# Kernel tuning notes

Hardware: AMD Instinct MI355X
Metric: run time of the kernel (lower is better)

## Reference

```python
import jax, jax.numpy as jnp
import numpy as np

N, D, P = 4096, 1024, 2048
TAU, ALPHA = 0.2, 0.8
GAMMA_EX, GAMMA_IN = 2.0, 1.6
EPS = 1e-8


def _cos_sim(e):
    # F.cosine_similarity(e[:,None], e[None,:], dim=2) == normalized rows matmul
    n = jnp.linalg.norm(e, axis=1, keepdims=True)
    en = e / jnp.maximum(n, EPS)
    return en @ en.T  # [N, N]


def setup_inputs() -> dict:
    key = jax.random.key(0)
    embeddings = jax.random.normal(key, (N, D), dtype=jnp.float32)
    # positive pairs: (0,1),(2,3),... (arange fill)
    pp = np.arange(2 * P).reshape(P, 2)
    pos_partner = np.arange(N)
    pos_partner[pp[:, 0]] = pp[:, 1]
    pos_partner[pp[:, 1]] = pp[:, 0]
    # negative pairs = all ordered (i,j), i!=j, minus ordered positive tuples,
    # enumerated row-major (deterministic stand-in for torch's set order).
    pos_m = np.zeros((N, N), dtype=bool)
    pos_m[pp[:, 0], pp[:, 1]] = True
    neg_m = ~np.eye(N, dtype=bool) & ~pos_m
    ii, jj = np.nonzero(neg_m)  # row-major order
    neg_partner = np.arange(N)
    neg_partner[ii] = jj
    neg_partner[jj] = ii  # processed[j] = ... overwrites after
    return {
        "embeddings": embeddings,
        "positive_pairs": jnp.asarray(pp, jnp.int32),
        "pos_partner": jnp.asarray(pos_partner, jnp.int32),
        "neg_partner": jnp.asarray(neg_partner, jnp.int32),
    }


def reference(embeddings, positive_pairs, pos_partner, neg_partner):
    pi, pj = positive_pairs[:, 0], positive_pairs[:, 1]
    # Beta(gamma,gamma) scalar mixing coefficients (dim_mixing=False)
    lam_pos = jax.random.beta(jax.random.key(1), GAMMA_EX, GAMMA_EX) + 1.0  # 'ex'
    lam_neg = jax.random.beta(jax.random.key(2), GAMMA_IN, GAMMA_IN)        # 'in'

    orig = _cos_sim(embeddings)
    hp = _cos_sim(lam_pos * embeddings + (1.0 - lam_pos) * embeddings[pos_partner])
    hn = _cos_sim(lam_neg * embeddings + (1.0 - lam_neg) * embeddings[neg_partner])

    eye = jnp.eye(N, dtype=bool)
    pos_m = jnp.zeros((N, N), dtype=bool).at[pi, pj].set(True)  # ordered positives
    neg_m = ~eye & ~pos_m                                        # ordered negatives
    # pos replacement first, then neg replacement overwrites (faithful ordering)
    sim = jnp.where(pos_m | pos_m.T, hp, orig)
    sim = jnp.where(neg_m | neg_m.T, hn, sim)

    # ----- compute_loss (stage='train': quantile hard-negative mining) -----
    mask = eye | pos_m | pos_m.T
    exp_sim = jnp.exp(sim / TAU)
    exp_masked = jnp.where(mask, 0.0, exp_sim)
    pos_ij = exp_sim[pi, pj]
    pos_ji = exp_sim[pj, pi]
    exp_i = exp_masked[pi]  # [P, N]
    exp_j = exp_masked[pj]
    thr_i = jnp.quantile(exp_i, ALPHA, axis=1, keepdims=True)
    thr_j = jnp.quantile(exp_j, ALPHA, axis=1, keepdims=True)
    sum_i = jnp.where(exp_i >= thr_i, exp_i, 0.0).sum(axis=1)
    sum_j = jnp.where(exp_j >= thr_j, exp_j, 0.0).sum(axis=1)
    loss_ij = -jnp.log(pos_ij / (pos_ij + sum_i))
    loss_ji = -jnp.log(pos_ji / (pos_ji + sum_j))
    return (loss_ij + loss_ji).sum() / (2 * P)
```

## Files before the change

kernel.cpp:

```cpp
#include <hip/hip_runtime.h>
#include <hip/hip_bf16.h>

#define NN 4096
#define DD 1024
constexpr float LAM = 0.45f;
constexpr float INV_TAU = 5.0f;
constexpr int KSEL = 820;
constexpr unsigned KEY_BASE = 0x3B80u;
constexpr int NBINS = 2048;

typedef __attribute__((ext_vector_type(8))) short bf16x8;
typedef __attribute__((ext_vector_type(4))) float f32x4;

__device__ inline void async_copy16(const ushort* g, ushort* l) {
    __builtin_amdgcn_global_load_lds(
        (const __attribute__((address_space(1))) void*)g,
        (__attribute__((address_space(3))) void*)l, 16, 0, 0);
}

#define BAR() do { asm volatile("" ::: "memory"); __builtin_amdgcn_s_barrier(); \
                   asm volatile("" ::: "memory"); } while (0)

__global__ __launch_bounds__(256) void mixnorm_kernel(const float* __restrict__ E,
                                                      const int* __restrict__ negp,
                                                      ushort* __restrict__ U) {
    int r = blockIdx.x, t = threadIdx.x;
    int p = negp[r];
    const float a = LAM, b = 1.0f - LAM;
    float4 x = ((const float4*)(E + (size_t)r * DD))[t];
    float4 y = ((const float4*)(E + (size_t)p * DD))[t];
    float4 m;
    m.x = a * x.x + b * y.x;
    m.y = a * x.y + b * y.y;
    m.z = a * x.z + b * y.z;
    m.w = a * x.w + b * y.w;
    float ss = m.x * m.x + m.y * m.y + m.z * m.z + m.w * m.w;
    #pragma unroll
    for (int off = 32; off > 0; off >>= 1) ss += __shfl_down(ss, off, 64);
    __shared__ float part[4];
    if ((t & 63) == 0) part[t >> 6] = ss;
    __syncthreads();
    float tot = part[0] + part[1] + part[2] + part[3];
    float inv = 1.0f / fmaxf(sqrtf(tot), 1e-8f);
    ushort4 o;
    o.x = __bfloat16_as_ushort(__float2bfloat16(m.x * inv));
    o.y = __bfloat16_as_ushort(__float2bfloat16(m.y * inv));
    o.z = __bfloat16_as_ushort(__float2bfloat16(m.z * inv));
    o.w = __bfloat16_as_ushort(__float2bfloat16(m.w * inv));
    ((ushort4*)(U + (size_t)r * DD))[t] = o;
}

__global__ __launch_bounds__(512, 2) void gemm_exp_kernel(const ushort* __restrict__ U,
                                                          ushort* __restrict__ Z) {
    __shared__ ushort sm[49152];
    const int t = threadIdx.x;
    const int w = t >> 6, l = t & 63;
    const int wr = w >> 2, wc = w & 3;

    const int bid = blockIdx.x;
    const int swz = (bid & 7) * 32 + (bid >> 3);
    const int by = swz >> 4, bx = swz & 15;

    const int srow = t >> 2;
    const int scs = (t & 3) ^ (srow & 3);
    const size_t sgo = (size_t)srow * DD + scs * 8;
    const ushort* gA = U + (size_t)(by * 256) * DD;
    const ushort* gB = U + (size_t)(bx * 256) * DD;
    #define STAGEH(dst_u, gX, h, k2) \
        async_copy16(gX + (size_t)(h) * 128 * DD + sgo + (k2), sm + (dst_u) + t * 8)

    const int rA = l & 15;
    const int sA8 = (((l >> 4) ^ (l & 3))) * 8;
    const int brow = (wc & 1) * 64 + rA;
    const int bh = (wc >> 1) * 4096;

    f32x4 acc[8][4];
    #pragma unroll
    for (int i = 0; i < 8; i++)
        #pragma unroll
        for (int j = 0; j < 4; j++) acc[i][j] = (f32x4){0.f, 0.f, 0.f, 0.f};

    STAGEH(0,             gA, 0, 0);   STAGEH(4096,          gA, 1, 0);
    STAGEH(8192,          gB, 0, 0);   STAGEH(12288,         gB, 1, 0);
    STAGEH(16384 + 0,     gA, 0, 32);  STAGEH(16384 + 4096,  gA, 1, 32);
    STAGEH(16384 + 8192,  gB, 0, 32);  STAGEH(16384 + 12288, gB, 1, 32);

    int bb = 0, tb = 2;
    for (int kt = 0; kt < 32; kt++) {
        const int k2 = (kt + 2) * 32;
        const ushort* Ab = sm + bb * 16384 + wr * 4096;
        const ushort* Bb = sm + bb * 16384 + 8192 + bh;
        ushort* tbu = (ushort*)0;
        const bool st = (kt <= 29);
        const int tbase = tb * 16384;

        if (kt == 31) asm volatile("s_waitcnt vmcnt(0)" ::: "memory");
        else          asm volatile("s_waitcnt vmcnt(4)" ::: "memory");
        if (st) { STAGEH(tbase, gA, 0, k2); STAGEH(tbase + 4096, gA, 1, k2); }
        BAR();
        {
            bf16x8 bfr[4], af[4];
            #pragma unroll
            for (int j = 0; j < 4; j++)
                bfr[j] = *(const bf16x8*)(Bb + (brow + j * 16) * 32 + sA8);
            #pragma unroll
            for (int i = 0; i < 4; i++)
                af[i] = *(const bf16x8*)(Ab + (rA + i * 16) * 32 + sA8);
            __builtin_amdgcn_s_setprio(1);
            #pragma unroll
            for (int i = 0; i < 4; i++)
                #pragma unroll
                for (int j = 0; j < 4; j++)
                    acc[i][j] = __builtin_amdgcn_mfma_f32_16x16x32_bf16(af[i], bfr[j], acc[i][j], 0, 0, 0);
            __builtin_amdgcn_s_setprio(0);
            BAR();

            #pragma unroll
            for (int i = 0; i < 4; i++)
                af[i] = *(const bf16x8*)(Ab + (rA + (4 + i) * 16) * 32 + sA8);
            if (st) { STAGEH(tbase + 8192, gB, 0, k2); STAGEH(tbase + 12288, gB, 1, k2); }
            BAR();
            __builtin_amdgcn_s_setprio(1);
            #pragma unroll
            for (int i = 0; i < 4; i++)
                #pragma unroll
                for (int j = 0; j < 4; j++)
                    acc[4 + i][j] = __builtin_amdgcn_mfma_f32_16x16x32_bf16(af[i], bfr[j], acc[4 + i][j], 0, 0, 0);
            __builtin_amdgcn_s_setprio(0);
            BAR();
        }
        (void)tbu;
        bb = (bb == 2) ? 0 : bb + 1;
        tb = (tb == 2) ? 0 : tb + 1;
    }
    #undef STAGEH

    #pragma unroll
    for (int i = 0; i < 8; i++) {
        __syncthreads();
        #pragma unroll
        for (int j = 0; j < 4; j++)
            #pragma unroll
            for (int rg = 0; rg < 4; rg++) {
                float v = __expf(acc[i][j][rg] * INV_TAU);
                ushort hv = __bfloat16_as_ushort(__float2bfloat16(v));
                int lrow = wr * 16 + ((l >> 4) << 2) + rg;
                int lcol = wc * 64 + j * 16 + rA;
                sm[lrow * 256 + lcol] = hv;
            }
        __syncthreads();
        #pragma unroll
        for (int q = 0; q < 2; q++) {
            int n = q * 512 + t;
            int row = n >> 5;
            int c = n & 31;
            int grow = by * 256 + (row >> 4) * 128 + i * 16 + (row & 15);
            const uint4* src = (const uint4*)(sm + row * 256 + c * 8);
            uint4* dst = (uint4*)(Z + (size_t)grow * NN + bx * 256 + c * 8);
            *dst = *src;
        }
    }
}

__global__ __launch_bounds__(256) void rowloss_kernel(const ushort* __restrict__ Z,
                                                      const int* __restrict__ posp,
                                                      float* __restrict__ loss) {
    const int t = threadIdx.x, w = t >> 6, l = t & 63;
    const int r = blockIdx.x * 4 + w;
    const int p = posp[r];
    const uint4* zr = (const uint4*)(Z + (size_t)r * NN);

    const float posv = __uint_as_float(((unsigned)Z[(size_t)r * NN + p]) << 16);

    unsigned ko[32];
    #pragma unroll
    for (int c = 0; c < 8; c++) {
        uint4 v = zr[c * 64 + l];
        unsigned wd[4] = {v.x, v.y, v.z, v.w};
        const int cb = (c * 64 + l) * 8;
        #pragma unroll
        for (int q = 0; q < 4; q++) {
            int c0 = cb + 2 * q, c1 = c0 + 1;
            unsigned x = wd[q];
            unsigned klo = (c0 == p || c0 == r) ? 0u : (x & 0xFFFFu);
            unsigned khi = (c1 == p || c1 == r) ? 0u : (x >> 16);
            ko[c * 4 + q] = klo | (khi << 16) | 0x80008000u;
        }
    }

    unsigned lo_b = KEY_BASE, hi_b = KEY_BASE + NBINS;
    #pragma unroll 1
    for (int it = 0; it < 11; it++) {
        unsigned mid = (lo_b + hi_b) >> 1;
        unsigned mm = mid | (mid << 16);
        unsigned a = 0;
        #pragma unroll
        for (int i = 0; i < 32; i++)
            a += ((ko[i] - mm) >> 15) & 0x10001u;
        #pragma unroll
        for (int d = 1; d < 64; d <<= 1) a += __shfl_xor(a, d, 64);
        unsigned c = (a & 0xFFFFu) + (a >> 16);
        bool ge = (c >= (unsigned)KSEL);
        lo_b = ge ? mid : lo_b;
        hi_b = ge ? hi_b : mid;
    }
    const unsigned thr = lo_b;

    float s0 = 0.f, s1 = 0.f;
    #pragma unroll
    for (int i = 0; i < 32; i++) {
        unsigned x = ko[i] & 0x7FFF7FFFu;
        unsigned klo = x & 0xFFFFu;
        unsigned khi = x >> 16;
        float vlo = __uint_as_float(klo << 16);
        float vhi = __uint_as_float(x & 0xFFFF0000u);
        s0 += (klo >= thr) ? vlo : 0.f;
        s1 += (khi >= thr) ? vhi : 0.f;
    }
    float s = s0 + s1;
    #pragma unroll
    for (int d = 1; d < 64; d <<= 1) s += __shfl_xor(s, d, 64);
    if (l == 0) loss[r] = log1pf(s / posv);
}

__global__ __launch_bounds__(256) void finalize_kernel(const float* __restrict__ loss,
                                                       unsigned* __restrict__ out) {
    __shared__ float part[4];
    const int t = threadIdx.x, w = t >> 6, l = t & 63;
    float s = 0.f;
    #pragma unroll
    for (int q = 0; q < 4; q++) {
        float4 v = ((const float4*)loss)[t * 4 + q];
        s += (v.x + v.y) + (v.z + v.w);
    }
    #pragma unroll
    for (int off = 32; off > 0; off >>= 1) s += __shfl_down(s, off, 64);
    if (l == 0) part[w] = s;
    __syncthreads();
    if (t == 0) {
        float v = (part[0] + part[1] + part[2] + part[3]) * (1.0f / 4096.0f);
        unsigned short bits = __bfloat16_as_ushort(__float2bfloat16(v));
        *out = ((unsigned)bits << 16) | (unsigned)bits;
    }
}

extern "C" void kernel_launch(void* const* d_in, const int* in_sizes, int n_in,
                              void* d_out, int out_size, void* d_ws, size_t ws_size,
                              hipStream_t stream) {
    const float* E = (const float*)d_in[0];
    const int* posp = (const int*)d_in[2];
    const int* negp = (const int*)d_in[3];

    float* loss = (float*)d_ws;
    ushort* U = (ushort*)((char*)d_ws + 16384);
    ushort* Z = (ushort*)((char*)d_ws + 16384 + (size_t)NN * DD * 2);

    mixnorm_kernel<<<NN, 256, 0, stream>>>(E, negp, U);
    gemm_exp_kernel<<<256, 512, 0, stream>>>(U, Z);
    rowloss_kernel<<<NN / 4, 256, 0, stream>>>(Z, posp, loss);
    finalize_kernel<<<1, 256, 0, stream>>>(loss, (unsigned*)d_out);
}
```

Baseline: 127.3 us.

## Exploit Gram matrix symmetry by computing lower-triangular tiles and mirroring output

The similarity GEMM now computes only the lower-triangular tiles of U·Uᵀ. It uses 128x256 tiles, and a triangular index mapping turns block IDs into tile row and column. Each tile writes its exp values both in place and transposed, so the full Z matrix is still produced, with about half the MFMA and operand-load work. The cost is narrow 64-byte transposed global stores, an extra LDS transpose buffer, smaller per-block tiles with less reuse, and a small sqrt/loop search per block.

```diff
diff --git a/kernel.cpp b/kernel.cpp
--- a/kernel.cpp
+++ b/kernel.cpp
@@ -20,6 +20,11 @@
 
 #define BAR() do { asm volatile("" ::: "memory"); __builtin_amdgcn_s_barrier(); \
                    asm volatile("" ::: "memory"); } while (0)
+
+__device__ inline int tricum(int r) {
+    int m = r >> 1;
+    return (r & 1) ? (m + 1) * (m + 1) : m * m + m;
+}
 
 __global__ __launch_bounds__(256) void mixnorm_kernel(const float* __restrict__ E,
                                                       const int* __restrict__ negp,
@@ -52,63 +57,64 @@
 
 __global__ __launch_bounds__(512, 2) void gemm_exp_kernel(const ushort* __restrict__ U,
                                                           ushort* __restrict__ Z) {
-    __shared__ ushort sm[49152];
+    __shared__ ushort sm[36864];
     const int t = threadIdx.x;
     const int w = t >> 6, l = t & 63;
     const int wr = w >> 2, wc = w & 3;
 
     const int bid = blockIdx.x;
-    const int swz = (bid & 7) * 32 + (bid >> 3);
-    const int by = swz >> 4, bx = swz & 15;
+    const int swz = (bid & 7) * 34 + (bid >> 3);
+    int rs = (int)(2.0f * sqrtf((float)swz + 1.0f));
+    rs = rs > 31 ? 31 : rs;
+    while (rs < 31 && tricum(rs + 1) <= swz) rs++;
+    while (rs > 0 && tricum(rs) > swz) rs--;
+    const int cs = swz - tricum(rs);
+    const int row0 = rs * 128, col0 = cs * 256;
 
     const int srow = t >> 2;
     const int scs = (t & 3) ^ (srow & 3);
     const size_t sgo = (size_t)srow * DD + scs * 8;
-    const ushort* gA = U + (size_t)(by * 256) * DD;
-    const ushort* gB = U + (size_t)(bx * 256) * DD;
-    #define STAGEH(dst_u, gX, h, k2) \
-        async_copy16(gX + (size_t)(h) * 128 * DD + sgo + (k2), sm + (dst_u) + t * 8)
+    const ushort* gA = U + (size_t)row0 * DD;
+    const ushort* gB = U + (size_t)col0 * DD;
+    #define STAGEA(bu, k2) async_copy16(gA + sgo + (k2), sm + (bu) + t * 8)
+    #define STAGEB(bu, h, k2) \
+        async_copy16(gB + (size_t)(h) * 128 * DD + sgo + (k2), sm + (bu) + 4096 + (h) * 4096 + t * 8)
 
     const int rA = l & 15;
-    const int sA8 = (((l >> 4) ^ (l & 3))) * 8;
-    const int brow = (wc & 1) * 64 + rA;
-    const int bh = (wc >> 1) * 4096;
-
-    f32x4 acc[8][4];
-    #pragma unroll
-    for (int i = 0; i < 8; i++)
+    const int sA8 = ((l >> 4) ^ (l & 3)) * 8;
+
+    f32x4 acc[4][4];
+    #pragma unroll
+    for (int i = 0; i < 4; i++)
         #pragma unroll
         for (int j = 0; j < 4; j++) acc[i][j] = (f32x4){0.f, 0.f, 0.f, 0.f};
 
-    STAGEH(0,             gA, 0, 0);   STAGEH(4096,          gA, 1, 0);
-    STAGEH(8192,          gB, 0, 0);   STAGEH(12288,         gB, 1, 0);
-    STAGEH(16384 + 0,     gA, 0, 32);  STAGEH(16384 + 4096,  gA, 1, 32);
-    STAGEH(16384 + 8192,  gB, 0, 32);  STAGEH(16384 + 12288, gB, 1, 32);
+    STAGEA(0, 0);      STAGEB(0, 0, 0);      STAGEB(0, 1, 0);
+    STAGEA(12288, 32); STAGEB(12288, 0, 32); STAGEB(12288, 1, 32);
 
     int bb = 0, tb = 2;
     for (int kt = 0; kt < 32; kt++) {
         const int k2 = (kt + 2) * 32;
-        const ushort* Ab = sm + bb * 16384 + wr * 4096;
-        const ushort* Bb = sm + bb * 16384 + 8192 + bh;
-        ushort* tbu = (ushort*)0;
         const bool st = (kt <= 29);
-        const int tbase = tb * 16384;
+        const int tbase = tb * 12288;
+        const ushort* Ab = sm + bb * 12288 + (wr * 64) * 32;
+        const ushort* Bb = sm + bb * 12288 + 4096 + (wc * 64) * 32;
 
         if (kt == 31) asm volatile("s_waitcnt vmcnt(0)" ::: "memory");
-        else          asm volatile("s_waitcnt vmcnt(4)" ::: "memory");
-        if (st) { STAGEH(tbase, gA, 0, k2); STAGEH(tbase + 4096, gA, 1, k2); }
+        else          asm volatile("s_waitcnt vmcnt(3)" ::: "memory");
+        if (st) STAGEA(tbase, k2);
         BAR();
         {
             bf16x8 bfr[4], af[4];
             #pragma unroll
             for (int j = 0; j < 4; j++)
-                bfr[j] = *(const bf16x8*)(Bb + (brow + j * 16) * 32 + sA8);
-            #pragma unroll
-            for (int i = 0; i < 4; i++)
+                bfr[j] = *(const bf16x8*)(Bb + (rA + j * 16) * 32 + sA8);
+            #pragma unroll
+            for (int i = 0; i < 2; i++)
                 af[i] = *(const bf16x8*)(Ab + (rA + i * 16) * 32 + sA8);
             __builtin_amdgcn_s_setprio(1);
             #pragma unroll
-            for (int i = 0; i < 4; i++)
+            for (int i = 0; i < 2; i++)
                 #pragma unroll
                 for (int j = 0; j < 4; j++)
                     acc[i][j] = __builtin_amdgcn_mfma_f32_16x16x32_bf16(af[i], bfr[j], acc[i][j], 0, 0, 0);
@@ -116,48 +122,61 @@
             BAR();
 
             #pragma unroll
-            for (int i = 0; i < 4; i++)
-                af[i] = *(const bf16x8*)(Ab + (rA + (4 + i) * 16) * 32 + sA8);
-            if (st) { STAGEH(tbase + 8192, gB, 0, k2); STAGEH(tbase + 12288, gB, 1, k2); }
+            for (int i = 2; i < 4; i++)
+                af[i] = *(const bf16x8*)(Ab + (rA + i * 16) * 32 + sA8);
+            if (st) { STAGEB(tbase, 0, k2); STAGEB(tbase, 1, k2); }
             BAR();
             __builtin_amdgcn_s_setprio(1);
             #pragma unroll
-            for (int i = 0; i < 4; i++)
+            for (int i = 2; i < 4; i++)
                 #pragma unroll
                 for (int j = 0; j < 4; j++)
-                    acc[4 + i][j] = __builtin_amdgcn_mfma_f32_16x16x32_bf16(af[i], bfr[j], acc[4 + i][j], 0, 0, 0);
+                    acc[i][j] = __builtin_amdgcn_mfma_f32_16x16x32_bf16(af[i], bfr[j], acc[i][j], 0, 0, 0);
             __builtin_amdgcn_s_setprio(0);
             BAR();
         }
-        (void)tbu;
         bb = (bb == 2) ? 0 : bb + 1;
         tb = (tb == 2) ? 0 : tb + 1;
     }
-    #undef STAGEH
-
-    #pragma unroll
-    for (int i = 0; i < 8; i++) {
+    #undef STAGEA
+    #undef STAGEB
+
+    ushort* smv = sm;
+    ushort* smT = sm + 8192;
+    #pragma unroll
+    for (int h = 0; h < 4; h++) {
         __syncthreads();
-        #pragma unroll
-        for (int j = 0; j < 4; j++)
-            #pragma unroll
-            for (int rg = 0; rg < 4; rg++) {
-                float v = __expf(acc[i][j][rg] * INV_TAU);
-                ushort hv = __bfloat16_as_ushort(__float2bfloat16(v));
-                int lrow = wr * 16 + ((l >> 4) << 2) + rg;
-                int lcol = wc * 64 + j * 16 + rA;
-                sm[lrow * 256 + lcol] = hv;
-            }
+        if (wr == (h >> 1)) {
+            #pragma unroll
+            for (int i2 = 0; i2 < 2; i2++)
+                #pragma unroll
+                for (int j = 0; j < 4; j++)
+                    #pragma unroll
+                    for (int rg = 0; rg < 4; rg++) {
+                        float v = __expf(acc[(h & 1) * 2 + i2][j][rg] * INV_TAU);
+                        ushort hv = __bfloat16_as_ushort(__float2bfloat16(v));
+                        int lrow = i2 * 16 + ((l >> 4) << 2) + rg;
+                        int lcol = wc * 64 + j * 16 + rA;
+                        smv[lrow * 256 + lcol] = hv;
+                        smT[lcol * 48 + lrow] = hv;
+                    }
+        }
         __syncthreads();
         #pragma unroll
         for (int q = 0; q < 2; q++) {
             int n = q * 512 + t;
-            int row = n >> 5;
-            int c = n & 31;
-            int grow = by * 256 + (row >> 4) * 128 + i * 16 + (row & 15);
-            const uint4* src = (const uint4*)(sm + row * 256 + c * 8);
-            uint4* dst = (uint4*)(Z + (size_t)grow * NN + bx * 256 + c * 8);
+            int row = n >> 5, c = n & 31;
+            const uint4* src = (const uint4*)(smv + row * 256 + c * 8);
+            uint4* dst = (uint4*)(Z + (size_t)(row0 + h * 32 + row) * NN + col0 + c * 8);
             *dst = *src;
+        }
+        #pragma unroll
+        for (int q = 0; q < 2; q++) {
+            int n = q * 512 + t;
+            int mr = n >> 2, mc = n & 3;
+            const uint4* srcT = (const uint4*)(smT + mr * 48 + mc * 8);
+            uint4* dstT = (uint4*)(Z + (size_t)(col0 + mr) * NN + row0 + h * 32 + mc * 8);
+            *dstT = *srcT;
         }
     }
 }
@@ -256,7 +275,7 @@
     ushort* Z = (ushort*)((char*)d_ws + 16384 + (size_t)NN * DD * 2);
 
     mixnorm_kernel<<<NN, 256, 0, stream>>>(E, negp, U);
-    gemm_exp_kernel<<<256, 512, 0, stream>>>(U, Z);
+    gemm_exp_kernel<<<272, 512, 0, stream>>>(U, Z);
     rowloss_kernel<<<NN / 4, 256, 0, stream>>>(Z, posp, loss);
     finalize_kernel<<<1, 256, 0, stream>>>(loss, (unsigned*)d_out);
 }
```

Result: no change. 127.1 us (-0.1%).
